# Performance work log

Hardware: AMD Instinct MI355X
Metric: run time of the kernel (lower is better)

## Reference

```python
import jax, jax.numpy as jnp
import numpy as np

B, L, D, E = 32, 1024, 1024, 100  # batch, seq len, encoded_num, max_entities
Q_MAX = 200  # question tokens occupy [0, q_q_len); entities start after Q_MAX


def setup_inputs() -> dict:
    key = jax.random.key(0)
    k1, k2, k3, k4, k5, k6 = jax.random.split(key, 6)
    q_enc = jax.random.normal(k1, (B, L, D), dtype=jnp.float32)
    hint = jax.random.normal(k2, (B, L, 1), dtype=jnp.float32)
    q_q_len = jax.random.randint(k3, (B,), 150, Q_MAX + 1, dtype=jnp.int32)
    # entity ranges: entity e of batch b spans tokens (r0+1 .. r1-1), 3..7 tokens each,
    # laid out non-overlapping after the question region
    lens = np.asarray(jax.random.randint(k4, (B, E), 4, 9))  # r1 - r0
    starts = np.broadcast_to(Q_MAX + np.arange(E)[None, :] * 8, (B, E))
    entity_ranges = jnp.asarray(np.stack([starts, starts + lens], axis=-1), dtype=jnp.int32)
    W_attn = jax.random.normal(k5, (D + 1, D), dtype=jnp.float32) * 0.02  # nn.Linear(D, D+1)
    b_attn = jnp.zeros((D + 1,), jnp.float32)
    none_entity = jax.random.normal(k6, (1, D), dtype=jnp.float32) * 0.02
    return dict(q_enc=q_enc, hint=hint, W_attn=W_attn, b_attn=b_attn,
                none_entity=none_entity, q_q_len=q_q_len, entity_ranges=entity_ranges)


def reference(q_enc, hint, W_attn, b_attn, none_entity, q_q_len, entity_ranges):
    pos = jnp.arange(L)
    r0 = entity_ranges[..., 0]  # [B, E]
    r1 = entity_ranges[..., 1]
    # torch slice q_enc[b, r0+1:r1, :]  ->  mask pos in (r0, r1)
    ent_mask = ((pos[None, None, :] > r0[..., None]) &
                (pos[None, None, :] < r1[..., None])).astype(q_enc.dtype)  # [B, E, L]
    # ragged gather + segment-sum (zero-padding then sum == masked sum)
    encoded_entity = jnp.einsum('bel,bld->bed', ent_mask, q_enc)  # [B, E, D]
    encoded_entity = jnp.concatenate(
        [encoded_entity, jnp.broadcast_to(none_entity[None], (B, 1, D))], axis=1)  # [B, E+1, D]
    ent_proj = encoded_entity @ W_attn.T + b_attn  # [B, E+1, D+1]
    qv = jnp.concatenate([q_enc, hint], axis=-1)  # question_vectors with hint feature, [B, L, D+1]
    scores = jnp.einsum('blf,bef->ble', qv, ent_proj)  # [B, L, E+1]
    co_att = jax.nn.softmax(scores, axis=-1)
    # original only computes rows :q_q_len[b]; mask padded question rows to zero
    qmask = (pos[None, :] < q_q_len[:, None]).astype(co_att.dtype)[..., None]
    co_att = co_att * qmask
    att = jnp.minimum(jnp.sum(co_att, axis=1), 1.0)[:, :-1]  # clamp(max=1), drop none-entity col
    return att, co_att
```

## Files before the change

### kernel.cpp

```cpp
#include <hip/hip_runtime.h>
#include <hip/hip_bf16.h>

typedef unsigned short u16;
typedef __attribute__((ext_vector_type(8))) short short8;
typedef __attribute__((ext_vector_type(4))) float f32x4;

#define B_ 32
#define L_ 1024
#define D_ 1024
#define E_ 100
#define E1_ 101
#define M2_ (B_ * E1_)
#define M2P_ 3328
#define QBLK_ 16
#define NT3_ 13
#define ZROW0_ (NT3_ * QBLK_)
#define NZF_ 640
#define NPREP_ (M2_ + 1024 + NZF_)

#define MFMA16(a, b, c) __builtin_amdgcn_mfma_f32_16x16x32_bf16((a), (b), (c), 0, 0, 0)

__device__ __forceinline__ void split2(float x, u16& h, u16& l) {
    __hip_bfloat16 bh = __float2bfloat16(x);
    float r = x - __bfloat162float(bh);
    __hip_bfloat16 bl = __float2bfloat16(r);
    h = __builtin_bit_cast(u16, bh);
    l = __builtin_bit_cast(u16, bl);
}

__device__ __forceinline__ void gload16(const void* g, void* l) {
    __builtin_amdgcn_global_load_lds(
        (const __attribute__((address_space(1))) unsigned int*)g,
        (__attribute__((address_space(3))) unsigned int*)l, 16, 0, 0);
}

__global__ __launch_bounds__(256) void k_prep(const float* __restrict__ q_enc,
                                              const float* __restrict__ none_ent,
                                              const float* __restrict__ W,
                                              const float* __restrict__ bias,
                                              const int* __restrict__ ranges,
                                              u16* __restrict__ enc_hi, u16* __restrict__ enc_lo,
                                              u16* __restrict__ w_hi, u16* __restrict__ w_lo,
                                              float* __restrict__ ep_last,
                                              float* __restrict__ co_att) {
    __shared__ float red4[4];
    int u = blockIdx.x;
    int t = threadIdx.x, c = t * 4;
    if (u < M2_) {
        int b = u / E1_, e = u - b * E1_;
        float4 acc;
        if (e == E_) {
            acc = *(const float4*)&none_ent[c];
        } else {
            acc = make_float4(0.f, 0.f, 0.f, 0.f);
            int r0 = ranges[(b * E_ + e) * 2 + 0];
            int r1 = ranges[(b * E_ + e) * 2 + 1];
            for (int l = r0 + 1; l < r1; ++l) {
                float4 v = *(const float4*)&q_enc[((size_t)b * L_ + l) * D_ + c];
                acc.x += v.x; acc.y += v.y; acc.z += v.z; acc.w += v.w;
            }
        }
        union { u16 uu[4]; float2 f; } ph, pl;
        split2(acc.x, ph.uu[0], pl.uu[0]); split2(acc.y, ph.uu[1], pl.uu[1]);
        split2(acc.z, ph.uu[2], pl.uu[2]); split2(acc.w, ph.uu[3], pl.uu[3]);
        *(float2*)&enc_hi[(size_t)u * 1024 + c] = ph.f;
        *(float2*)&enc_lo[(size_t)u * 1024 + c] = pl.f;
        const float* w1k = W + (size_t)1024 * 1024;
        float4 wv = *(const float4*)&w1k[c];
        float s = acc.x * wv.x + acc.y * wv.y + acc.z * wv.z + acc.w * wv.w;
        #pragma unroll
        for (int off = 32; off; off >>= 1) s += __shfl_down(s, off);
        if ((t & 63) == 0) red4[t >> 6] = s;
        __syncthreads();
        if (t == 0) ep_last[u] = red4[0] + red4[1] + red4[2] + red4[3] + bias[1024];
    } else if (u < M2_ + 1024) {
        int r = u - M2_;
        float4 v = *(const float4*)&W[(size_t)r * 1024 + c];
        union { u16 uu[4]; float2 f; } ph, pl;
        split2(v.x, ph.uu[0], pl.uu[0]); split2(v.y, ph.uu[1], pl.uu[1]);
        split2(v.z, ph.uu[2], pl.uu[2]); split2(v.w, ph.uu[3], pl.uu[3]);
        *(float2*)&w_hi[(size_t)r * 1024 + c] = ph.f;
        *(float2*)&w_lo[(size_t)r * 1024 + c] = pl.f;
    } else {
        int zu = u - M2_ - 1024;
        int b = zu / 20, part = zu % 20;
        float4* base = (float4*)&co_att[((size_t)b * L_ + ZROW0_) * E1_];
        const int n4 = (L_ - ZROW0_) * E1_ / 4;
        float4 z = make_float4(0.f, 0.f, 0.f, 0.f);
        for (int i = part * 256 + t; i < n4; i += 20 * 256)
            base[i] = z;
    }
}

__global__ __launch_bounds__(256, 4) void k_entproj(const u16* __restrict__ A_hi, const u16* __restrict__ A_lo,
                                                    const u16* __restrict__ B_hi, const u16* __restrict__ B_lo,
                                                    const float* __restrict__ bias,
                                                    u16* __restrict__ ep_hi, u16* __restrict__ ep_lo) {
    __shared__ __attribute__((aligned(16))) u16 Ah[64 * 64], Al[64 * 64], Bh[64 * 64], Bl[64 * 64];
    int tid = threadIdx.x;
    int m0 = blockIdx.y * 64, n0 = blockIdx.x * 64;
    int w = tid >> 6, lane = tid & 63, lr = lane & 15, lg = lane >> 4;
    int wr = w >> 1, wc = w & 1;
    f32x4 zero = {0.f, 0.f, 0.f, 0.f};
    f32x4 acc[2][2] = {{zero, zero}, {zero, zero}};
    for (int k0 = 0; k0 < 1024; k0 += 64) {
        #pragma unroll
        for (int j = 0; j < 2; ++j) {
            int slot = w * 128 + j * 64 + lane;
            int r = slot >> 3, s = slot & 7;
            int g = (s ^ (r & 7)) << 3;
            size_t ga = (size_t)(m0 + r) * 1024 + k0 + g;
            size_t gb = (size_t)(n0 + r) * 1024 + k0 + g;
            int ld = (w * 128 + j * 64) * 8;
            gload16(&A_hi[ga], &Ah[ld]);
            gload16(&A_lo[ga], &Al[ld]);
            gload16(&B_hi[gb], &Bh[ld]);
            gload16(&B_lo[gb], &Bl[ld]);
        }
        __syncthreads();
        #pragma unroll
        for (int half = 0; half < 2; ++half) {
            int sk = half * 4 + lg;
            short8 a_h[2], a_l[2], b_h[2], b_l[2];
            #pragma unroll
            for (int mf = 0; mf < 2; ++mf) {
                int R = wr * 32 + mf * 16 + lr;
                int ad = R * 64 + ((sk ^ (R & 7)) << 3);
                a_h[mf] = __builtin_bit_cast(short8, *(const float4*)&Ah[ad]);
                a_l[mf] = __builtin_bit_cast(short8, *(const float4*)&Al[ad]);
            }
            #pragma unroll
            for (int nf = 0; nf < 2; ++nf) {
                int R = wc * 32 + nf * 16 + lr;
                int ad = R * 64 + ((sk ^ (R & 7)) << 3);
                b_h[nf] = __builtin_bit_cast(short8, *(const float4*)&Bh[ad]);
                b_l[nf] = __builtin_bit_cast(short8, *(const float4*)&Bl[ad]);
            }
            #pragma unroll
            for (int mf = 0; mf < 2; ++mf)
                #pragma unroll
                for (int nf = 0; nf < 2; ++nf) {
                    acc[mf][nf] = MFMA16(a_h[mf], b_h[nf], acc[mf][nf]);
                    acc[mf][nf] = MFMA16(a_h[mf], b_l[nf], acc[mf][nf]);
                    acc[mf][nf] = MFMA16(a_l[mf], b_h[nf], acc[mf][nf]);
                }
        }
        __syncthreads();
    }
    #pragma unroll
    for (int mf = 0; mf < 2; ++mf)
        #pragma unroll
        for (int nf = 0; nf < 2; ++nf)
            #pragma unroll
            for (int reg = 0; reg < 4; ++reg) {
                int m = m0 + wr * 32 + mf * 16 + lg * 4 + reg;
                if (m < M2_) {
                    int n = n0 + wc * 32 + nf * 16 + lr;
                    float v = acc[mf][nf][reg] + bias[n];
                    u16 h, l;
                    split2(v, h, l);
                    ep_hi[(size_t)m * 1024 + n] = h;
                    ep_lo[(size_t)m * 1024 + n] = l;
                }
            }
}

__global__ __launch_bounds__(256, 3) void k_scores(const float* __restrict__ q_enc,
                                                   const float* __restrict__ hint,
                                                   const u16* __restrict__ ep_hi, const u16* __restrict__ ep_lo,
                                                   const float* __restrict__ ep_last,
                                                   const int* __restrict__ qlen,
                                                   float* __restrict__ co_att,
                                                   float* __restrict__ partial) {
    __shared__ __attribute__((aligned(16))) u16 Ah[16 * 64], Al[16 * 64], Bh[128 * 64], Bl[128 * 64];
    __shared__ float Ss[16 * 113];
    __shared__ float red[QBLK_][16];
    int id = blockIdx.x;
    int b = id & 31, mt = id >> 5, l0 = mt * QBLK_;
    int tid = threadIdx.x;
    int qn = qlen[b];
    if (l0 >= qn) {
        float* base = &co_att[((size_t)b * L_ + l0) * E1_];
        float4 z = make_float4(0.f, 0.f, 0.f, 0.f);
        for (int i = tid; i < QBLK_ * E1_ / 4; i += 256)
            *(float4*)&base[i * 4] = z;
        for (int e = tid; e < E1_; e += 256)
            partial[((size_t)b * NT3_ + mt) * E1_ + e] = 0.f;
        return;
    }
    int w = tid >> 6, lane = tid & 63, lr = lane & 15, lg = lane >> 4;
    int nb = w * 2, nc = (w == 3) ? 1 : 2;
    int sb = w * 256;
    f32x4 zero = {0.f, 0.f, 0.f, 0.f};
    f32x4 acc[2] = {zero, zero};
    for (int k0 = 0; k0 < 1024; k0 += 64) {
        {
            #pragma unroll
            for (int j = 0; j < 4; ++j) {
                int slot = sb + j * 64 + lane;
                int r = slot >> 3, s = slot & 7;
                int g = (s ^ (r & 7)) << 3;
                size_t gb = ((size_t)b * E1_ + r) * 1024 + k0 + g;
                int ld = (sb + j * 64) * 8;
                gload16(&ep_hi[gb], &Bh[ld]);
                gload16(&ep_lo[gb], &Bl[ld]);
            }
        }
        if (tid < 128) {
            int r = tid >> 3, s = tid & 7;
            const float* src = &q_enc[((size_t)b * L_ + l0 + r) * D_ + k0 + s * 8];
            float4 x0 = *(const float4*)src, x1 = *(const float4*)(src + 4);
            float xs[8] = {x0.x, x0.y, x0.z, x0.w, x1.x, x1.y, x1.z, x1.w};
            short8 hv, lv;
            #pragma unroll
            for (int j = 0; j < 8; ++j) {
                u16 hh, ll;
                split2(xs[j], hh, ll);
                hv[j] = (short)hh; lv[j] = (short)ll;
            }
            int dst = r * 64 + ((s ^ (r & 7)) << 3);
            *(float4*)&Ah[dst] = __builtin_bit_cast(float4, hv);
            *(float4*)&Al[dst] = __builtin_bit_cast(float4, lv);
        }
        __syncthreads();
        #pragma unroll
        for (int ks = 0; ks < 2; ++ks) {
            int sk = ks * 4 + lg;
            int adA = lr * 64 + ((sk ^ (lr & 7)) << 3);
            short8 ah = __builtin_bit_cast(short8, *(const float4*)&Ah[adA]);
            short8 al = __builtin_bit_cast(short8, *(const float4*)&Al[adA]);
            #pragma unroll
            for (int nf = 0; nf < 2; ++nf) {
                if (nf < nc) {
                    int rB = (nb + nf) * 16 + lr;
                    int adB = rB * 64 + ((sk ^ (rB & 7)) << 3);
                    short8 bh = __builtin_bit_cast(short8, *(const float4*)&Bh[adB]);
                    short8 bl = __builtin_bit_cast(short8, *(const float4*)&Bl[adB]);
                    acc[nf] = MFMA16(ah, bh, acc[nf]);
                    acc[nf] = MFMA16(ah, bl, acc[nf]);
                    acc[nf] = MFMA16(al, bh, acc[nf]);
                }
            }
        }
        __syncthreads();
    }
    #pragma unroll
    for (int nf = 0; nf < 2; ++nf)
        if (nf < nc) {
            #pragma unroll
            for (int reg = 0; reg < 4; ++reg)
                Ss[(lg * 4 + reg) * 113 + (nb + nf) * 16 + lr] = acc[nf][reg];
        }
    __syncthreads();
    int l = tid & 15, eg = tid >> 4;
    float h = hint[(size_t)b * L_ + l0 + l];
    float sc[7];
    #pragma unroll
    for (int j = 0; j < 7; ++j) {
        int e = eg + 16 * j;
        sc[j] = (e < E1_) ? (Ss[l * 113 + e] + h * ep_last[b * E1_ + e]) : -3.4e38f;
    }
    float mloc = -3.4e38f;
    #pragma unroll
    for (int j = 0; j < 7; ++j) mloc = fmaxf(mloc, sc[j]);
    red[l][eg] = mloc;
    __syncthreads();
    float m = red[l][0];
    #pragma unroll
    for (int k = 1; k < 16; ++k) m = fmaxf(m, red[l][k]);
    __syncthreads();
    float p[7];
    float sloc = 0.f;
    #pragma unroll
    for (int j = 0; j < 7; ++j) {
        p[j] = 0.f;
        if (eg + 16 * j < E1_) { p[j] = __expf(sc[j] - m); sloc += p[j]; }
    }
    red[l][eg] = sloc;
    __syncthreads();
    float ssum = 0.f;
    #pragma unroll
    for (int k = 0; k < 16; ++k) ssum += red[l][k];
    float inv = 1.f / ssum;
    bool valid = (l0 + l) < qn;
    float maskv = valid ? inv : 0.f;
    float* row = &co_att[((size_t)b * L_ + l0 + l) * E1_];
    #pragma unroll
    for (int j = 0; j < 7; ++j) {
        int e = eg + 16 * j;
        if (e < E1_) row[e] = p[j] * maskv;
    }
    #pragma unroll
    for (int j = 0; j < 7; ++j) {
        int e = eg + 16 * j;
        float v = (e < E1_) ? p[j] * maskv : 0.f;
        v += __shfl_xor(v, 1);  v += __shfl_xor(v, 2);
        v += __shfl_xor(v, 4);  v += __shfl_xor(v, 8);
        if ((tid & 15) == 0 && e < E1_)
            partial[((size_t)b * NT3_ + mt) * E1_ + e] = v;
    }
}

__global__ __launch_bounds__(256) void k_final(const float* __restrict__ partial,
                                               float* __restrict__ att) {
    int i = blockIdx.x * 256 + threadIdx.x;
    if (i >= B_ * E_) return;
    int b = i / E_, e = i % E_;
    float s = 0.f;
    #pragma unroll
    for (int k = 0; k < NT3_; ++k) s += partial[((size_t)b * NT3_ + k) * E1_ + e];
    att[i] = fminf(s, 1.f);
}

extern "C" void kernel_launch(void* const* d_in, const int* in_sizes, int n_in,
                              void* d_out, int out_size, void* d_ws, size_t ws_size,
                              hipStream_t stream) {
    const float* q_enc    = (const float*)d_in[0];
    const float* hint     = (const float*)d_in[1];
    const float* W        = (const float*)d_in[2];
    const float* bias     = (const float*)d_in[3];
    const float* none_ent = (const float*)d_in[4];
    const int*   qlen     = (const int*)d_in[5];
    const int*   ranges   = (const int*)d_in[6];

    float* att    = (float*)d_out;
    float* co_att = att + (size_t)B_ * E_;

    u16* enc_hi = (u16*)d_ws;
    u16* enc_lo = enc_hi + (size_t)M2P_ * 1024;
    u16* w_hi   = enc_lo + (size_t)M2P_ * 1024;
    u16* w_lo   = w_hi + (size_t)1024 * 1024;
    u16* ep_hi  = w_lo + (size_t)1024 * 1024;
    u16* ep_lo  = ep_hi + (size_t)M2P_ * 1024;
    float* ep_last = (float*)(ep_lo + (size_t)M2P_ * 1024);
    float* part    = ep_last + M2P_;

    k_prep<<<NPREP_, 256, 0, stream>>>(q_enc, none_ent, W, bias, ranges,
                                       enc_hi, enc_lo, w_hi, w_lo, ep_last, co_att);
    k_entproj<<<dim3(16, 52), 256, 0, stream>>>(enc_hi, enc_lo, w_hi, w_lo, bias, ep_hi, ep_lo);
    k_scores<<<B_ * NT3_, 256, 0, stream>>>(q_enc, hint, ep_hi, ep_lo, ep_last, qlen, co_att, part);
    k_final<<<13, 256, 0, stream>>>(part, att);
}
```

Baseline: 76.46 us.

## Load MFMA operands directly from global memory in score kernel, dropping LDS staging

The score kernel no longer stages the question and entity-projection tiles through shared memory with barriers. Each wave now reads its own A and B fragments straight from global memory into registers, splitting the fp32 inputs into bf16 hi/lo in place, with a 4x unrolled K loop. This removes the LDS traffic and the per-iteration __syncthreads, and the launch bound rises to 4 blocks per SM. In exchange, each wave re-reads and re-splits the same question rows redundantly across the 4 waves, and the global accesses are strided per lane and no longer coalesced.

```diff
diff --git a/kernel.cpp b/kernel.cpp
--- a/kernel.cpp
+++ b/kernel.cpp
@@ -165,14 +165,13 @@
             }
 }
 
-__global__ __launch_bounds__(256, 3) void k_scores(const float* __restrict__ q_enc,
+__global__ __launch_bounds__(256, 4) void k_scores(const float* __restrict__ q_enc,
                                                    const float* __restrict__ hint,
                                                    const u16* __restrict__ ep_hi, const u16* __restrict__ ep_lo,
                                                    const float* __restrict__ ep_last,
                                                    const int* __restrict__ qlen,
                                                    float* __restrict__ co_att,
                                                    float* __restrict__ partial) {
-    __shared__ __attribute__((aligned(16))) u16 Ah[16 * 64], Al[16 * 64], Bh[128 * 64], Bl[128 * 64];
     __shared__ float Ss[16 * 113];
     __shared__ float red[QBLK_][16];
     int id = blockIdx.x;
@@ -190,59 +189,34 @@
     }
     int w = tid >> 6, lane = tid & 63, lr = lane & 15, lg = lane >> 4;
     int nb = w * 2, nc = (w == 3) ? 1 : 2;
-    int sb = w * 256;
     f32x4 zero = {0.f, 0.f, 0.f, 0.f};
     f32x4 acc[2] = {zero, zero};
-    for (int k0 = 0; k0 < 1024; k0 += 64) {
-        {
-            #pragma unroll
-            for (int j = 0; j < 4; ++j) {
-                int slot = sb + j * 64 + lane;
-                int r = slot >> 3, s = slot & 7;
-                int g = (s ^ (r & 7)) << 3;
-                size_t gb = ((size_t)b * E1_ + r) * 1024 + k0 + g;
-                int ld = (sb + j * 64) * 8;
-                gload16(&ep_hi[gb], &Bh[ld]);
-                gload16(&ep_lo[gb], &Bl[ld]);
-            }
-        }
-        if (tid < 128) {
-            int r = tid >> 3, s = tid & 7;
-            const float* src = &q_enc[((size_t)b * L_ + l0 + r) * D_ + k0 + s * 8];
-            float4 x0 = *(const float4*)src, x1 = *(const float4*)(src + 4);
-            float xs[8] = {x0.x, x0.y, x0.z, x0.w, x1.x, x1.y, x1.z, x1.w};
-            short8 hv, lv;
-            #pragma unroll
-            for (int j = 0; j < 8; ++j) {
-                u16 hh, ll;
-                split2(xs[j], hh, ll);
-                hv[j] = (short)hh; lv[j] = (short)ll;
-            }
-            int dst = r * 64 + ((s ^ (r & 7)) << 3);
-            *(float4*)&Ah[dst] = __builtin_bit_cast(float4, hv);
-            *(float4*)&Al[dst] = __builtin_bit_cast(float4, lv);
-        }
-        __syncthreads();
-        #pragma unroll
-        for (int ks = 0; ks < 2; ++ks) {
-            int sk = ks * 4 + lg;
-            int adA = lr * 64 + ((sk ^ (lr & 7)) << 3);
-            short8 ah = __builtin_bit_cast(short8, *(const float4*)&Ah[adA]);
-            short8 al = __builtin_bit_cast(short8, *(const float4*)&Al[adA]);
-            #pragma unroll
-            for (int nf = 0; nf < 2; ++nf) {
-                if (nf < nc) {
-                    int rB = (nb + nf) * 16 + lr;
-                    int adB = rB * 64 + ((sk ^ (rB & 7)) << 3);
-                    short8 bh = __builtin_bit_cast(short8, *(const float4*)&Bh[adB]);
-                    short8 bl = __builtin_bit_cast(short8, *(const float4*)&Bl[adB]);
-                    acc[nf] = MFMA16(ah, bh, acc[nf]);
-                    acc[nf] = MFMA16(ah, bl, acc[nf]);
-                    acc[nf] = MFMA16(al, bh, acc[nf]);
-                }
-            }
-        }
-        __syncthreads();
+    const float* qrow = &q_enc[((size_t)b * L_ + l0 + lr) * D_ + lg * 8];
+    const u16* eph0 = &ep_hi[((size_t)b * E1_ + nb * 16 + lr) * 1024 + lg * 8];
+    const u16* epl0 = &ep_lo[((size_t)b * E1_ + nb * 16 + lr) * 1024 + lg * 8];
+    #pragma unroll 4
+    for (int t = 0; t < 32; ++t) {
+        int k = t * 32;
+        float4 x0 = *(const float4*)(qrow + k);
+        float4 x1 = *(const float4*)(qrow + k + 4);
+        float xs[8] = {x0.x, x0.y, x0.z, x0.w, x1.x, x1.y, x1.z, x1.w};
+        short8 ah, al;
+        #pragma unroll
+        for (int j = 0; j < 8; ++j) {
+            u16 hh, ll;
+            split2(xs[j], hh, ll);
+            ah[j] = (short)hh; al[j] = (short)ll;
+        }
+        #pragma unroll
+        for (int nf = 0; nf < 2; ++nf) {
+            if (nf < nc) {
+                short8 bh = *(const short8*)(eph0 + (size_t)nf * 16 * 1024 + k);
+                short8 bl = *(const short8*)(epl0 + (size_t)nf * 16 * 1024 + k);
+                acc[nf] = MFMA16(ah, bh, acc[nf]);
+                acc[nf] = MFMA16(ah, bl, acc[nf]);
+                acc[nf] = MFMA16(al, bh, acc[nf]);
+            }
+        }
     }
     #pragma unroll
     for (int nf = 0; nf < 2; ++nf)
```

New measurement: 99.46 us. 30.1% more time.
